# Optimization experiments

Hardware: AMD Instinct MI355X
Metric: run time of the kernel (lower is better)

## Reference

```python
import jax, jax.numpy as jnp
import numpy as np

NUM_HEADS = 16
EMBED_DIM = 1024
HEAD_DIM = EMBED_DIM // NUM_HEADS
SCALE = HEAD_DIM * -0.5  # faithful to source: multiplicative, negative


def setup_inputs() -> dict:
    key = jax.random.key(0)
    kx, kq, kk, kv, ko = jax.random.split(key, 5)
    B, S, E = 2, 2048, EMBED_DIM
    std = 1.0 / np.sqrt(E)
    return {
        "x": jax.random.normal(kx, (B, S, E), dtype=jnp.float32),
        "Wq": jax.random.normal(kq, (E, E), dtype=jnp.float32) * std,
        "Wk": jax.random.normal(kk, (E, E), dtype=jnp.float32) * std,
        "Wv": jax.random.normal(kv, (E, E), dtype=jnp.float32) * std,
        "Wo": jax.random.normal(ko, (E, E), dtype=jnp.float32) * std,
    }


def reference(x, Wq, Wk, Wv, Wo):
    B, S, E = x.shape
    H, D = NUM_HEADS, HEAD_DIM
    # nn.Linear(bias=False): y = x @ W.T
    q = (x @ Wq.T).reshape(B, S, H, D).transpose(0, 2, 1, 3)  # unused downstream (faithful to source)
    k = (x @ Wk.T).reshape(B, S, H, D).transpose(0, 2, 1, 3)  # [B,H,S,D]
    v = (x @ Wv.T).reshape(B, S, H, D).transpose(0, 2, 1, 3)
    # Source bug reproduced: logits = K @ V^T, scaled by head_dim * -0.5
    logits = jnp.einsum('bhsd,bhtd->bhst', k, v) * SCALE  # [B,H,S,S]
    attn = jax.nn.softmax(logits, axis=-1)
    out = jnp.einsum('bhst,bhtd->bhsd', attn, v)  # [B,H,S,D]
    out = out.transpose(0, 2, 1, 3).reshape(B, S, E)
    return out @ Wo.T
```

## Files before the change

kernel.cpp:

```cpp
#include <hip/hip_runtime.h>
#include <math.h>

#define B_ 2
#define S_ 2048
#define E_ 1024
#define H_ 16
#define D_ 64
#define M_ (B_ * S_)
#define SC2 (-46.166241308446828f)

typedef unsigned short u16;
typedef _Float16 f16;
typedef __attribute__((ext_vector_type(8))) _Float16 f16x8;
typedef __attribute__((ext_vector_type(2))) __fp16 fp16x2_n;
typedef __attribute__((ext_vector_type(16))) float f32x16;

static __device__ __forceinline__ f32x16 mfma_h(f16x8 a, f16x8 b, f32x16 c) {
    return __builtin_amdgcn_mfma_f32_32x32x16_f16(a, b, c, 0, 0, 0);
}
static __device__ __forceinline__ u16 f16bits(f16 h) {
    union { f16 h; u16 u; } c; c.h = h; return c.u;
}
static __device__ __forceinline__ unsigned pack2(u16 a, u16 b) {
    return (unsigned)a | ((unsigned)b << 16);
}
static __device__ __forceinline__ unsigned pkrtz(float a, float b) {
    fp16x2_n h = __builtin_amdgcn_cvt_pkrtz(a, b);
    unsigned u; __builtin_memcpy(&u, &h, 4); return u;
}
static __device__ __forceinline__ void pl32swap(unsigned &a, unsigned &b) {
    asm volatile("v_permlane32_swap_b32 %0, %1" : "+v"(a), "+v"(b));
}
#define ROWMAP(r, hh) (((r) & 3) + ((((r) >> 2)) << 3) + ((hh) << 2))

__global__ __launch_bounds__(256)
void convert_split(const float* __restrict__ x, const float* __restrict__ Wk,
                   const float* __restrict__ Wv, const float* __restrict__ Wo,
                   u16* __restrict__ Xh, u16* __restrict__ Xl,
                   u16* __restrict__ Wkh, u16* __restrict__ Wkl,
                   u16* __restrict__ Wvh, u16* __restrict__ Wvl,
                   u16* __restrict__ Woh)
{
    const int blk = blockIdx.x;
    const float* src; u16 *dh, *dl; int base; float sc = 1.0f; bool wantlo = true;
    if (blk < 4096)      { src = x;  dh = Xh;  dl = Xl;  base = blk; }
    else if (blk < 5120) { src = Wk; dh = Wkh; dl = Wkl; base = blk - 4096; sc = SC2; }
    else if (blk < 6144) { src = Wv; dh = Wvh; dl = Wvl; base = blk - 5120; }
    else                 { src = Wo; dh = Woh; dl = Woh; base = blk - 6144; wantlo = false; }
    const size_t off = ((size_t)base * 256 + threadIdx.x) * 4;
    const float4 v = *(const float4*)(src + off);
    const float f[4] = {v.x * sc, v.y * sc, v.z * sc, v.w * sc};
    u16 h4[4], l4[4];
#pragma unroll
    for (int i = 0; i < 4; ++i) {
        const f16 h = (f16)f[i];
        h4[i] = f16bits(h);
        l4[i] = f16bits((f16)(f[i] - (float)h));
    }
    *(uint2*)(dh + off) = make_uint2(pack2(h4[0], h4[1]), pack2(h4[2], h4[3]));
    if (wantlo)
        *(uint2*)(dl + off) = make_uint2(pack2(l4[0], l4[1]), pack2(l4[2], l4[3]));
}

#define CSB 1032
#define ARR (4 * CSB)

template<int MODE>
__global__ __launch_bounds__(512, 2)
void gemm_f(const u16* __restrict__ Ah_, const u16* __restrict__ Al_,
            const u16* __restrict__ Bkh_, const u16* __restrict__ Bkl_,
            const u16* __restrict__ Bvh_, const u16* __restrict__ Bvl_,
            u16* __restrict__ Khg, u16* __restrict__ Klg,
            u16* __restrict__ Vhg, u16* __restrict__ Vtg,
            float* __restrict__ Cout)
{
    constexpr int NARR = (MODE == 0 ? 6 : 2);
    constexpr int SSZ = (NARR * ARR > 16384 ? NARR * ARR : 16384);
    __shared__ u16 stage[SSZ];

    const int tid = threadIdx.x;
    const int w = tid >> 6, l31 = tid & 31, hh = (tid >> 5) & 1;
    const int wt = w & 3, ws = w >> 2;
    const int wm = (wt >> 1) << 6, wn = (wt & 1) << 6;
    const int m0 = blockIdx.y * 128, n0 = blockIdx.x * 128;
    const int ch8 = (ws << 1) + hh;

    const int sr = tid >> 2, sch = tid & 3;
    const size_t gA = (size_t)(m0 + sr) * E_ + (sch << 3);
    const size_t gB = (size_t)(n0 + sr) * E_ + (sch << 3);
    const int slo = sch * CSB + sr * 8;

    f32x16 acc1[2][2], acc2[2][2];
#pragma unroll
    for (int mt = 0; mt < 2; ++mt)
#pragma unroll
        for (int nt = 0; nt < 2; ++nt)
#pragma unroll
            for (int r = 0; r < 16; ++r) {
                acc1[mt][nt][r] = 0.f;
                if constexpr (MODE == 0) acc2[mt][nt][r] = 0.f;
            }

    f16x8 pf[NARR];
    auto load_tile = [&](int k0) {
        pf[0] = *(const f16x8*)(Ah_ + gA + k0);
        if constexpr (MODE == 0) {
            pf[1] = *(const f16x8*)(Al_ + gA + k0);
            pf[2] = *(const f16x8*)(Bkh_ + gB + k0);
            pf[3] = *(const f16x8*)(Bkl_ + gB + k0);
            pf[4] = *(const f16x8*)(Bvh_ + gB + k0);
            pf[5] = *(const f16x8*)(Bvl_ + gB + k0);
        } else {
            pf[1] = *(const f16x8*)(Bkh_ + gB + k0);
        }
    };
    auto store_tile = [&]() {
#pragma unroll
        for (int a = 0; a < NARR; ++a)
            *(f16x8*)&stage[a * ARR + slo] = pf[a];
    };

    load_tile(0);
    for (int it = 0; it < 32; ++it) {
        store_tile();
        __syncthreads();
        if (it + 1 < 32) load_tile((it + 1) << 5);

        const int co = ch8 * CSB;
        f16x8 xh[2], xl[2];
#pragma unroll
        for (int mt = 0; mt < 2; ++mt) {
            const int off = co + (wm + (mt << 5) + l31) * 8;
            xh[mt] = *(const f16x8*)&stage[0 * ARR + off];
            if constexpr (MODE == 0)
                xl[mt] = *(const f16x8*)&stage[1 * ARR + off];
        }
#pragma unroll
        for (int nt = 0; nt < 2; ++nt) {
            const int ro = co + (wn + (nt << 5) + l31) * 8;
            if constexpr (MODE == 0) {
                const f16x8 bkh = *(const f16x8*)&stage[2 * ARR + ro];
                const f16x8 bkl = *(const f16x8*)&stage[3 * ARR + ro];
                const f16x8 bvh = *(const f16x8*)&stage[4 * ARR + ro];
                const f16x8 bvl = *(const f16x8*)&stage[5 * ARR + ro];
#pragma unroll
                for (int mt = 0; mt < 2; ++mt) {
                    acc1[mt][nt] = mfma_h(xh[mt], bkh, acc1[mt][nt]);
                    acc1[mt][nt] = mfma_h(xh[mt], bkl, acc1[mt][nt]);
                    acc1[mt][nt] = mfma_h(xl[mt], bkh, acc1[mt][nt]);
                    acc2[mt][nt] = mfma_h(xh[mt], bvh, acc2[mt][nt]);
                    acc2[mt][nt] = mfma_h(xh[mt], bvl, acc2[mt][nt]);
                    acc2[mt][nt] = mfma_h(xl[mt], bvh, acc2[mt][nt]);
                }
            } else {
                const f16x8 bh = *(const f16x8*)&stage[1 * ARR + ro];
#pragma unroll
                for (int mt = 0; mt < 2; ++mt)
                    acc1[mt][nt] = mfma_h(xh[mt], bh, acc1[mt][nt]);
            }
        }
        __syncthreads();
    }

    float* red = (float*)stage;
    constexpr int NR = (MODE == 0 ? 4 : 2);
#pragma unroll
    for (int rd = 0; rd < NR; ++rd) {
        const int mt = rd & 1;
        f32x16 (*A)[2] = (MODE == 0 && rd >= 2) ? acc2 : acc1;
        __syncthreads();
        if (ws == 1) {
#pragma unroll
            for (int nt = 0; nt < 2; ++nt)
#pragma unroll
                for (int r = 0; r < 16; ++r)
                    red[(((wt << 1) + nt) << 10) + (r << 6) + (hh << 5) + l31] = A[mt][nt][r];
        }
        __syncthreads();
        if (ws == 0) {
#pragma unroll
            for (int nt = 0; nt < 2; ++nt)
#pragma unroll
                for (int r = 0; r < 16; ++r)
                    A[mt][nt][r] += red[(((wt << 1) + nt) << 10) + (r << 6) + (hh << 5) + l31];
        }
    }
    if (ws != 0) return;

#pragma unroll
    for (int nt = 0; nt < 2; ++nt) {
        const int n = n0 + wn + (nt << 5) + l31;
        if constexpr (MODE == 1) {
#pragma unroll
            for (int mt = 0; mt < 2; ++mt)
#pragma unroll
                for (int r = 0; r < 16; ++r) {
                    const int m = m0 + wm + (mt << 5) + ROWMAP(r, hh);
                    Cout[(size_t)m * E_ + n] = acc1[mt][nt][r];
                }
        } else {
            const int hd = n >> 6, d = n & 63;
            const int b = m0 >> 11;
#pragma unroll
            for (int mt = 0; mt < 2; ++mt) {
                u16 vb16[16];
#pragma unroll
                for (int r = 0; r < 16; ++r) {
                    const int s = (m0 + wm + (mt << 5) + ROWMAP(r, hh)) & (S_ - 1);
                    const size_t ib = (((size_t)(b * H_ + hd) << 11) + s) * D_ + d;
                    const float kv = acc1[mt][nt][r];
                    const f16 kh = (f16)kv;
                    Khg[ib] = f16bits(kh);
                    Klg[ib] = f16bits((f16)(kv - (float)kh));
                    const f16 vh = (f16)acc2[mt][nt][r];
                    vb16[r] = f16bits(vh);
                    Vhg[ib] = vb16[r];
                }
                const size_t vtb = ((size_t)(b * H_ + hd) * D_ + d) << 11;
#pragma unroll
                for (int g = 0; g < 4; ++g) {
                    const int s0 = ((m0 + wm + (mt << 5)) & (S_ - 1)) + (g << 3) + (hh << 2);
                    *(uint2*)&Vtg[vtb + s0] =
                        make_uint2(pack2(vb16[4 * g], vb16[4 * g + 1]),
                                   pack2(vb16[4 * g + 2], vb16[4 * g + 3]));
                }
            }
        }
    }
}

#define CSA 520
#define VA  (8 * CSA)

__global__ __launch_bounds__(512, 2)
void attn_mfma(const u16* __restrict__ Kh, const u16* __restrict__ Kl,
               const u16* __restrict__ Vh, const u16* __restrict__ Vt,
               u16* __restrict__ Obuf)
{
    __shared__ u16 sV[4 * VA];

    const int tid = threadIdx.x;
    const int w = tid >> 6, l31 = tid & 31, hh = (tid >> 5) & 1;
    const int bh = blockIdx.y;
    const int sbase = blockIdx.x * 256 + (w << 5);
    const int sg = sbase + l31;

    f16x8 kfh[4], kfl[4];
    {
        const size_t kb = ((size_t)bh * S_ + sg) * D_;
#pragma unroll
        for (int ks = 0; ks < 4; ++ks) {
            const int db = (ks << 4) + (hh << 3);
            kfh[ks] = *(const f16x8*)(Kh + kb + db);
            kfl[ks] = *(const f16x8*)(Kl + kb + db);
        }
    }

    f32x16 oacc[2];
#pragma unroll
    for (int r = 0; r < 16; ++r) { oacc[0][r] = 0.f; oacc[1][r] = 0.f; }
    float m_i = -INFINITY, l_i = 0.f;

    const int rr = tid >> 3, cc = tid & 7;
    const size_t gn = ((size_t)bh * S_ + rr) * D_ + (cc << 3);
    const size_t gt = ((size_t)bh * D_ + rr) * S_ + (cc << 3);
    const int slo = cc * CSA + rr * 8;

    f16x8 pv[2];
    auto load_tile = [&](int it2) {
        const size_t t0 = (size_t)it2 << 6;
        pv[0] = *(const f16x8*)(Vh + gn + t0 * D_);
        pv[1] = *(const f16x8*)(Vt + gt + t0);
    };

    load_tile(0);
    *(f16x8*)&sV[slo] = pv[0];
    *(f16x8*)&sV[VA + slo] = pv[1];
    __syncthreads();

    for (int it = 0; it < 32; ++it) {
        const int vb = (it & 1) * (2 * VA);
        const int nb = ((it + 1) & 1) * (2 * VA);
        if (it + 1 < 32) load_tile(it + 1);

        f32x16 sta[2], stb[2];
#pragma unroll
        for (int r = 0; r < 16; ++r) {
            sta[0][r] = 0.f; sta[1][r] = 0.f;
            stb[0][r] = 0.f; stb[1][r] = 0.f;
        }
#pragma unroll
        for (int ks = 0; ks < 4; ++ks) {
            const int ch = (ks << 1) + hh;
#pragma unroll
            for (int mt = 0; mt < 2; ++mt) {
                const f16x8 av = *(const f16x8*)&sV[vb + ch * CSA + ((mt << 5) + l31) * 8];
                sta[mt] = mfma_h(av, kfh[ks], sta[mt]);
                stb[mt] = mfma_h(av, kfl[ks], stb[mt]);
            }
        }
#pragma unroll
        for (int mt = 0; mt < 2; ++mt)
#pragma unroll
            for (int r = 0; r < 16; ++r) sta[mt][r] += stb[mt][r];

        float tmax = -INFINITY;
#pragma unroll
        for (int mt = 0; mt < 2; ++mt)
#pragma unroll
            for (int r = 0; r < 16; ++r) tmax = fmaxf(tmax, sta[mt][r]);
        tmax = fmaxf(tmax, __shfl_xor(tmax, 32));
        const float mnew = fmaxf(m_i, tmax);
        const float alpha = __builtin_amdgcn_exp2f(m_i - mnew);
        m_i = mnew;
        const unsigned long long cmask = __ballot(tmax >= mnew - 30.f);

        if (cmask) {
            float rsum = 0.f;
#pragma unroll
            for (int mt = 0; mt < 2; ++mt)
#pragma unroll
                for (int r = 0; r < 16; ++r) {
                    const float p = __builtin_amdgcn_exp2f(sta[mt][r] - mnew);
                    sta[mt][r] = p;
                    rsum += p;
                }
            rsum += __shfl_xor(rsum, 32);
            l_i = l_i * alpha + rsum;

#pragma unroll
            for (int r = 0; r < 16; ++r) { oacc[0][r] *= alpha; oacc[1][r] *= alpha; }

            unsigned pa[2][4], pb[2][4];
#pragma unroll
            for (int mt = 0; mt < 2; ++mt)
#pragma unroll
                for (int q = 0; q < 4; ++q) {
                    pa[mt][q] = pkrtz(sta[mt][4 * q + 0], sta[mt][4 * q + 1]);
                    pb[mt][q] = pkrtz(sta[mt][4 * q + 2], sta[mt][4 * q + 3]);
                }

#pragma unroll
            for (int ks = 0; ks < 4; ++ks) {
                const int mt = ks >> 1, kk = ks & 1;
                unsigned w0 = pa[mt][2 * kk], w2v = pa[mt][2 * kk + 1];
                pl32swap(w0, w2v);
                unsigned w1 = pb[mt][2 * kk], w3v = pb[mt][2 * kk + 1];
                pl32swap(w1, w3v);
                union { unsigned u[4]; f16x8 v; } bw;
                bw.u[0] = w0; bw.u[1] = w1; bw.u[2] = w2v; bw.u[3] = w3v;
                const int ch = (ks << 1) + hh;
#pragma unroll
                for (int nt = 0; nt < 2; ++nt) {
                    const f16x8 vtf = *(const f16x8*)&sV[vb + VA + ch * CSA + ((nt << 5) + l31) * 8];
                    oacc[nt] = mfma_h(vtf, bw.v, oacc[nt]);
                }
            }
        }

        if (it + 1 < 32) {
            *(f16x8*)&sV[nb + slo] = pv[0];
            *(f16x8*)&sV[nb + VA + slo] = pv[1];
        }
        __syncthreads();
    }

    const float linv = (l_i > 0.f) ? (1.0f / l_i) : 0.f;
    const int b = bh >> 4;
    const int hd = bh & 15;
    u16* Or = Obuf + ((size_t)b * S_ + sg) * E_ + (hd << 6);
#pragma unroll
    for (int nt = 0; nt < 2; ++nt)
#pragma unroll
        for (int q = 0; q < 4; ++q) {
            const int d0 = (nt << 5) + (q << 3) + (hh << 2);
            u16 c[4];
#pragma unroll
            for (int j = 0; j < 4; ++j)
                c[j] = f16bits((f16)(oacc[nt][4 * q + j] * linv));
            *(uint2*)&Or[d0] = make_uint2(pack2(c[0], c[1]), pack2(c[2], c[3]));
        }
}

extern "C" void kernel_launch(void* const* d_in, const int* in_sizes, int n_in,
                              void* d_out, int out_size, void* d_ws, size_t ws_size,
                              hipStream_t stream)
{
    (void)in_sizes; (void)n_in; (void)out_size; (void)ws_size;
    const float* x  = (const float*)d_in[0];
    const float* Wk = (const float*)d_in[2];
    const float* Wv = (const float*)d_in[3];
    const float* Wo = (const float*)d_in[4];
    float* out = (float*)d_out;

    char* ws = (char*)d_ws;
    const size_t MB = 1u << 20;
    u16* Xh  = (u16*)(ws + 0 * MB);
    u16* Xl  = (u16*)(ws + 8 * MB);
    u16* Wkh = (u16*)(ws + 16 * MB);
    u16* Wkl = (u16*)(ws + 18 * MB);
    u16* Wvh = (u16*)(ws + 20 * MB);
    u16* Wvl = (u16*)(ws + 22 * MB);
    u16* Woh = (u16*)(ws + 24 * MB);
    u16* Kh  = (u16*)(ws + 26 * MB);
    u16* Kl  = (u16*)(ws + 34 * MB);
    u16* Vh  = (u16*)(ws + 42 * MB);
    u16* Vt  = (u16*)(ws + 50 * MB);
    u16* Obuf = Xl;

    convert_split<<<7168, 256, 0, stream>>>(x, Wk, Wv, Wo,
                                            Xh, Xl, Wkh, Wkl, Wvh, Wvl, Woh);
    gemm_f<0><<<dim3(E_ / 128, M_ / 128), 512, 0, stream>>>(
        Xh, Xl, Wkh, Wkl, Wvh, Wvl, Kh, Kl, Vh, Vt, nullptr);
    attn_mfma<<<dim3(S_ / 256, B_ * H_), 512, 0, stream>>>(Kh, Kl, Vh, Vt, Obuf);
    gemm_f<1><<<dim3(E_ / 128, M_ / 128), 512, 0, stream>>>(
        Obuf, Obuf, Woh, Woh, Woh, Woh,
        nullptr, nullptr, nullptr, nullptr, out);
}
```

Measured before the change: 218.7 us.

## Process two KV tiles per iteration, issuing both score MFMAs before softmax

The attention loop now loads and stores two 64-key V tiles per iteration instead of one double-buffered tile. It computes both score tiles back to back before running softmax and PV on each, so the MFMAs of the second tile can overlap the softmax of the first. This halves the loop trip count and gives the scheduler more independent work. The cost is two barriers per iteration around the store, so the prefetched pair lands in LDS only after compute finishes rather than through alternating buffers, plus higher register pressure from keeping four score accumulators live.

```diff
diff --git a/kernel.cpp b/kernel.cpp
--- a/kernel.cpp
+++ b/kernel.cpp
@@ -266,28 +266,27 @@
     const size_t gt = ((size_t)bh * D_ + rr) * S_ + (cc << 3);
     const int slo = cc * CSA + rr * 8;
 
-    f16x8 pv[2];
-    auto load_tile = [&](int it2) {
-        const size_t t0 = (size_t)it2 << 6;
-        pv[0] = *(const f16x8*)(Vh + gn + t0 * D_);
-        pv[1] = *(const f16x8*)(Vt + gt + t0);
-    };
-
-    load_tile(0);
-    *(f16x8*)&sV[slo] = pv[0];
-    *(f16x8*)&sV[VA + slo] = pv[1];
-    __syncthreads();
-
-    for (int it = 0; it < 32; ++it) {
-        const int vb = (it & 1) * (2 * VA);
-        const int nb = ((it + 1) & 1) * (2 * VA);
-        if (it + 1 < 32) load_tile(it + 1);
-
-        f32x16 sta[2], stb[2];
+    f16x8 pv[4];
+    auto load_pair = [&](int p) {
+        const size_t tE = (size_t)(2 * p) << 6;
+        const size_t tO = (size_t)(2 * p + 1) << 6;
+        pv[0] = *(const f16x8*)(Vh + gn + tE * D_);
+        pv[1] = *(const f16x8*)(Vt + gt + tE);
+        pv[2] = *(const f16x8*)(Vh + gn + tO * D_);
+        pv[3] = *(const f16x8*)(Vt + gt + tO);
+    };
+    auto store_pair = [&]() {
+        *(f16x8*)&sV[slo] = pv[0];
+        *(f16x8*)&sV[VA + slo] = pv[1];
+        *(f16x8*)&sV[2 * VA + slo] = pv[2];
+        *(f16x8*)&sV[3 * VA + slo] = pv[3];
+    };
+
+    auto ST = [&](int vb, f32x16 (&sa)[2], f32x16 (&sb)[2]) {
 #pragma unroll
         for (int r = 0; r < 16; ++r) {
-            sta[0][r] = 0.f; sta[1][r] = 0.f;
-            stb[0][r] = 0.f; stb[1][r] = 0.f;
+            sa[0][r] = 0.f; sa[1][r] = 0.f;
+            sb[0][r] = 0.f; sb[1][r] = 0.f;
         }
 #pragma unroll
         for (int ks = 0; ks < 4; ++ks) {
@@ -295,20 +294,23 @@
 #pragma unroll
             for (int mt = 0; mt < 2; ++mt) {
                 const f16x8 av = *(const f16x8*)&sV[vb + ch * CSA + ((mt << 5) + l31) * 8];
-                sta[mt] = mfma_h(av, kfh[ks], sta[mt]);
-                stb[mt] = mfma_h(av, kfl[ks], stb[mt]);
+                sa[mt] = mfma_h(av, kfh[ks], sa[mt]);
+                sb[mt] = mfma_h(av, kfl[ks], sb[mt]);
             }
         }
+    };
+
+    auto SMPV = [&](int vb, f32x16 (&sa)[2], f32x16 (&sb)[2]) {
 #pragma unroll
         for (int mt = 0; mt < 2; ++mt)
 #pragma unroll
-            for (int r = 0; r < 16; ++r) sta[mt][r] += stb[mt][r];
+            for (int r = 0; r < 16; ++r) sa[mt][r] += sb[mt][r];
 
         float tmax = -INFINITY;
 #pragma unroll
         for (int mt = 0; mt < 2; ++mt)
 #pragma unroll
-            for (int r = 0; r < 16; ++r) tmax = fmaxf(tmax, sta[mt][r]);
+            for (int r = 0; r < 16; ++r) tmax = fmaxf(tmax, sa[mt][r]);
         tmax = fmaxf(tmax, __shfl_xor(tmax, 32));
         const float mnew = fmaxf(m_i, tmax);
         const float alpha = __builtin_amdgcn_exp2f(m_i - mnew);
@@ -321,8 +323,8 @@
             for (int mt = 0; mt < 2; ++mt)
 #pragma unroll
                 for (int r = 0; r < 16; ++r) {
-                    const float p = __builtin_amdgcn_exp2f(sta[mt][r] - mnew);
-                    sta[mt][r] = p;
+                    const float p = __builtin_amdgcn_exp2f(sa[mt][r] - mnew);
+                    sa[mt][r] = p;
                     rsum += p;
                 }
             rsum += __shfl_xor(rsum, 32);
@@ -336,8 +338,8 @@
             for (int mt = 0; mt < 2; ++mt)
 #pragma unroll
                 for (int q = 0; q < 4; ++q) {
-                    pa[mt][q] = pkrtz(sta[mt][4 * q + 0], sta[mt][4 * q + 1]);
-                    pb[mt][q] = pkrtz(sta[mt][4 * q + 2], sta[mt][4 * q + 3]);
+                    pa[mt][q] = pkrtz(sa[mt][4 * q + 0], sa[mt][4 * q + 1]);
+                    pb[mt][q] = pkrtz(sa[mt][4 * q + 2], sa[mt][4 * q + 3]);
                 }
 
 #pragma unroll
@@ -357,12 +359,26 @@
                 }
             }
         }
-
-        if (it + 1 < 32) {
-            *(f16x8*)&sV[nb + slo] = pv[0];
-            *(f16x8*)&sV[nb + VA + slo] = pv[1];
-        }
-        __syncthreads();
+    };
+
+    load_pair(0);
+    store_pair();
+    __syncthreads();
+
+    for (int p = 0; p < 16; ++p) {
+        if (p + 1 < 16) load_pair(p + 1);
+
+        f32x16 saE[2], sbE[2], saO[2], sbO[2];
+        ST(0, saE, sbE);
+        ST(2 * VA, saO, sbO);
+        SMPV(0, saE, sbE);
+        SMPV(2 * VA, saO, sbO);
+
+        if (p + 1 < 16) {
+            __syncthreads();
+            store_pair();
+            __syncthreads();
+        }
     }
 
     const float linv = (l_i > 0.f) ? (1.0f / l_i) : 0.f;
```

New measurement: 227.8 us. 1.04x slower.

## Double GEMM block to 1024 threads with one M-subtile per wave

Applied to the files above, without the earlier changes.

The projection GEMM kernels now launch 1024 threads per block instead of 512. The 128x128 tile is split across 16 waves, so each wave owns a 32x128 slice and half as many accumulators. Tile loading is shared across the doubled thread count, with each half of the block loading either the hi or the lo arrays. This lowers per-thread register pressure and the number of loads per thread to raise parallelism and latency hiding. In exchange, each wave issues fewer MFMAs per LDS fragment read, and the launch bound of four 1024-thread blocks may force register spills or be unachievable.

```diff
diff --git a/kernel.cpp b/kernel.cpp
--- a/kernel.cpp
+++ b/kernel.cpp
@@ -66,7 +66,7 @@
 #define ARR (4 * CSB)
 
 template<int MODE>
-__global__ __launch_bounds__(512, 2)
+__global__ __launch_bounds__(1024, 4)
 void gemm_f(const u16* __restrict__ Ah_, const u16* __restrict__ Al_,
             const u16* __restrict__ Bkh_, const u16* __restrict__ Bkl_,
             const u16* __restrict__ Bvh_, const u16* __restrict__ Bvl_,
@@ -80,44 +80,47 @@
 
     const int tid = threadIdx.x;
     const int w = tid >> 6, l31 = tid & 31, hh = (tid >> 5) & 1;
-    const int wt = w & 3, ws = w >> 2;
-    const int wm = (wt >> 1) << 6, wn = (wt & 1) << 6;
+    const int wt = w & 7, ws = w >> 3;
+    const int wm = (wt >> 1) << 5, wn = (wt & 1) << 6;
     const int m0 = blockIdx.y * 128, n0 = blockIdx.x * 128;
     const int ch8 = (ws << 1) + hh;
 
-    const int sr = tid >> 2, sch = tid & 3;
+    const int sub = tid >> 9;
+    const int sidx = tid & 511;
+    const int sr = sidx >> 2, sch = sidx & 3;
     const size_t gA = (size_t)(m0 + sr) * E_ + (sch << 3);
     const size_t gB = (size_t)(n0 + sr) * E_ + (sch << 3);
     const int slo = sch * CSB + sr * 8;
 
-    f32x16 acc1[2][2], acc2[2][2];
-#pragma unroll
-    for (int mt = 0; mt < 2; ++mt)
-#pragma unroll
-        for (int nt = 0; nt < 2; ++nt)
-#pragma unroll
-            for (int r = 0; r < 16; ++r) {
-                acc1[mt][nt][r] = 0.f;
-                if constexpr (MODE == 0) acc2[mt][nt][r] = 0.f;
-            }
-
-    f16x8 pf[NARR];
+    f32x16 acc1[2], acc2[2];
+#pragma unroll
+    for (int nt = 0; nt < 2; ++nt)
+#pragma unroll
+        for (int r = 0; r < 16; ++r) {
+            acc1[nt][r] = 0.f;
+            if constexpr (MODE == 0) acc2[nt][r] = 0.f;
+        }
+
+    constexpr int NPF = (MODE == 0 ? 3 : 1);
+    f16x8 pf[NPF];
     auto load_tile = [&](int k0) {
-        pf[0] = *(const f16x8*)(Ah_ + gA + k0);
         if constexpr (MODE == 0) {
-            pf[1] = *(const f16x8*)(Al_ + gA + k0);
-            pf[2] = *(const f16x8*)(Bkh_ + gB + k0);
-            pf[3] = *(const f16x8*)(Bkl_ + gB + k0);
-            pf[4] = *(const f16x8*)(Bvh_ + gB + k0);
-            pf[5] = *(const f16x8*)(Bvl_ + gB + k0);
+            pf[0] = *(const f16x8*)((sub ? Al_ : Ah_) + gA + k0);
+            pf[1] = *(const f16x8*)((sub ? Bkl_ : Bkh_) + gB + k0);
+            pf[2] = *(const f16x8*)((sub ? Bvl_ : Bvh_) + gB + k0);
         } else {
-            pf[1] = *(const f16x8*)(Bkh_ + gB + k0);
+            pf[0] = sub ? *(const f16x8*)(Bkh_ + gB + k0)
+                        : *(const f16x8*)(Ah_ + gA + k0);
         }
     };
     auto store_tile = [&]() {
-#pragma unroll
-        for (int a = 0; a < NARR; ++a)
-            *(f16x8*)&stage[a * ARR + slo] = pf[a];
+        if constexpr (MODE == 0) {
+            *(f16x8*)&stage[(0 + sub) * ARR + slo] = pf[0];
+            *(f16x8*)&stage[(2 + sub) * ARR + slo] = pf[1];
+            *(f16x8*)&stage[(4 + sub) * ARR + slo] = pf[2];
+        } else {
+            *(f16x8*)&stage[sub * ARR + slo] = pf[0];
+        }
     };
 
     load_tile(0);
@@ -127,14 +130,10 @@
         if (it + 1 < 32) load_tile((it + 1) << 5);
 
         const int co = ch8 * CSB;
-        f16x8 xh[2], xl[2];
-#pragma unroll
-        for (int mt = 0; mt < 2; ++mt) {
-            const int off = co + (wm + (mt << 5) + l31) * 8;
-            xh[mt] = *(const f16x8*)&stage[0 * ARR + off];
-            if constexpr (MODE == 0)
-                xl[mt] = *(const f16x8*)&stage[1 * ARR + off];
-        }
+        const int off = co + (wm + l31) * 8;
+        const f16x8 xh = *(const f16x8*)&stage[0 * ARR + off];
+        f16x8 xl;
+        if constexpr (MODE == 0) xl = *(const f16x8*)&stage[1 * ARR + off];
 #pragma unroll
         for (int nt = 0; nt < 2; ++nt) {
             const int ro = co + (wn + (nt << 5) + l31) * 8;
@@ -143,20 +142,15 @@
                 const f16x8 bkl = *(const f16x8*)&stage[3 * ARR + ro];
                 const f16x8 bvh = *(const f16x8*)&stage[4 * ARR + ro];
                 const f16x8 bvl = *(const f16x8*)&stage[5 * ARR + ro];
-#pragma unroll
-                for (int mt = 0; mt < 2; ++mt) {
-                    acc1[mt][nt] = mfma_h(xh[mt], bkh, acc1[mt][nt]);
-                    acc1[mt][nt] = mfma_h(xh[mt], bkl, acc1[mt][nt]);
-                    acc1[mt][nt] = mfma_h(xl[mt], bkh, acc1[mt][nt]);
-                    acc2[mt][nt] = mfma_h(xh[mt], bvh, acc2[mt][nt]);
-                    acc2[mt][nt] = mfma_h(xh[mt], bvl, acc2[mt][nt]);
-                    acc2[mt][nt] = mfma_h(xl[mt], bvh, acc2[mt][nt]);
-                }
+                acc1[nt] = mfma_h(xh, bkh, acc1[nt]);
+                acc1[nt] = mfma_h(xh, bkl, acc1[nt]);
+                acc1[nt] = mfma_h(xl, bkh, acc1[nt]);
+                acc2[nt] = mfma_h(xh, bvh, acc2[nt]);
+                acc2[nt] = mfma_h(xh, bvl, acc2[nt]);
+                acc2[nt] = mfma_h(xl, bvh, acc2[nt]);
             } else {
                 const f16x8 bh = *(const f16x8*)&stage[1 * ARR + ro];
-#pragma unroll
-                for (int mt = 0; mt < 2; ++mt)
-                    acc1[mt][nt] = mfma_h(xh[mt], bh, acc1[mt][nt]);
+                acc1[nt] = mfma_h(xh, bh, acc1[nt]);
             }
         }
         __syncthreads();
@@ -166,23 +160,19 @@
     constexpr int NR = (MODE == 0 ? 4 : 2);
 #pragma unroll
     for (int rd = 0; rd < NR; ++rd) {
-        const int mt = rd & 1;
-        f32x16 (*A)[2] = (MODE == 0 && rd >= 2) ? acc2 : acc1;
+        const int ntr = rd & 1;
+        f32x16* A = (MODE == 0 && rd >= 2) ? &acc2[ntr] : &acc1[ntr];
         __syncthreads();
         if (ws == 1) {
 #pragma unroll
-            for (int nt = 0; nt < 2; ++nt)
-#pragma unroll
-                for (int r = 0; r < 16; ++r)
-                    red[(((wt << 1) + nt) << 10) + (r << 6) + (hh << 5) + l31] = A[mt][nt][r];
+            for (int r = 0; r < 16; ++r)
+                red[(wt << 10) + (r << 6) + (hh << 5) + l31] = (*A)[r];
         }
         __syncthreads();
         if (ws == 0) {
 #pragma unroll
-            for (int nt = 0; nt < 2; ++nt)
-#pragma unroll
-                for (int r = 0; r < 16; ++r)
-                    A[mt][nt][r] += red[(((wt << 1) + nt) << 10) + (r << 6) + (hh << 5) + l31];
+            for (int r = 0; r < 16; ++r)
+                (*A)[r] += red[(wt << 10) + (r << 6) + (hh << 5) + l31];
         }
     }
     if (ws != 0) return;
@@ -192,38 +182,33 @@
         const int n = n0 + wn + (nt << 5) + l31;
         if constexpr (MODE == 1) {
 #pragma unroll
-            for (int mt = 0; mt < 2; ++mt)
-#pragma unroll
-                for (int r = 0; r < 16; ++r) {
-                    const int m = m0 + wm + (mt << 5) + ROWMAP(r, hh);
-                    Cout[(size_t)m * E_ + n] = acc1[mt][nt][r];
-                }
+            for (int r = 0; r < 16; ++r) {
+                const int m = m0 + wm + ROWMAP(r, hh);
+                Cout[(size_t)m * E_ + n] = acc1[nt][r];
+            }
         } else {
             const int hd = n >> 6, d = n & 63;
             const int b = m0 >> 11;
-#pragma unroll
-            for (int mt = 0; mt < 2; ++mt) {
-                u16 vb16[16];
-#pragma unroll
-                for (int r = 0; r < 16; ++r) {
-                    const int s = (m0 + wm + (mt << 5) + ROWMAP(r, hh)) & (S_ - 1);
-                    const size_t ib = (((size_t)(b * H_ + hd) << 11) + s) * D_ + d;
-                    const float kv = acc1[mt][nt][r];
-                    const f16 kh = (f16)kv;
-                    Khg[ib] = f16bits(kh);
-                    Klg[ib] = f16bits((f16)(kv - (float)kh));
-                    const f16 vh = (f16)acc2[mt][nt][r];
-                    vb16[r] = f16bits(vh);
-                    Vhg[ib] = vb16[r];
-                }
-                const size_t vtb = ((size_t)(b * H_ + hd) * D_ + d) << 11;
-#pragma unroll
-                for (int g = 0; g < 4; ++g) {
-                    const int s0 = ((m0 + wm + (mt << 5)) & (S_ - 1)) + (g << 3) + (hh << 2);
-                    *(uint2*)&Vtg[vtb + s0] =
-                        make_uint2(pack2(vb16[4 * g], vb16[4 * g + 1]),
-                                   pack2(vb16[4 * g + 2], vb16[4 * g + 3]));
-                }
+            u16 vb16[16];
+#pragma unroll
+            for (int r = 0; r < 16; ++r) {
+                const int s = (m0 + wm + ROWMAP(r, hh)) & (S_ - 1);
+                const size_t ib = (((size_t)(b * H_ + hd) << 11) + s) * D_ + d;
+                const float kv = acc1[nt][r];
+                const f16 kh = (f16)kv;
+                Khg[ib] = f16bits(kh);
+                Klg[ib] = f16bits((f16)(kv - (float)kh));
+                const f16 vh = (f16)acc2[nt][r];
+                vb16[r] = f16bits(vh);
+                Vhg[ib] = vb16[r];
+            }
+            const size_t vtb = ((size_t)(b * H_ + hd) * D_ + d) << 11;
+#pragma unroll
+            for (int g = 0; g < 4; ++g) {
+                const int s0 = ((m0 + wm) & (S_ - 1)) + (g << 3) + (hh << 2);
+                *(uint2*)&Vtg[vtb + s0] =
+                    make_uint2(pack2(vb16[4 * g], vb16[4 * g + 1]),
+                               pack2(vb16[4 * g + 2], vb16[4 * g + 3]));
             }
         }
     }
@@ -410,10 +395,10 @@
 
     convert_split<<<7168, 256, 0, stream>>>(x, Wk, Wv, Wo,
                                             Xh, Xl, Wkh, Wkl, Wvh, Wvl, Woh);
-    gemm_f<0><<<dim3(E_ / 128, M_ / 128), 512, 0, stream>>>(
+    gemm_f<0><<<dim3(E_ / 128, M_ / 128), 1024, 0, stream>>>(
         Xh, Xl, Wkh, Wkl, Wvh, Wvl, Kh, Kl, Vh, Vt, nullptr);
     attn_mfma<<<dim3(S_ / 256, B_ * H_), 512, 0, stream>>>(Kh, Kl, Vh, Vt, Obuf);
-    gemm_f<1><<<dim3(E_ / 128, M_ / 128), 512, 0, stream>>>(
+    gemm_f<1><<<dim3(E_ / 128, M_ / 128), 1024, 0, stream>>>(
         Obuf, Obuf, Woh, Woh, Woh, Woh,
         nullptr, nullptr, nullptr, nullptr, out);
 }
```

New measurement: 224.1 us. +2.5%, slower.
